# Kernel optimization log

Hardware: AMD Instinct MI355X
Metric: run time of the kernel (lower is better)

Reference implementation:

```python
import jax, jax.numpy as jnp
import numpy as np

NUM_HEADS = 8


def _attn(q, k, v, scale):
    # q: [B,H,Nq,d], k/v: [B,H,Nk,d]
    a = jax.nn.softmax(jnp.einsum('bhqd,bhkd->bhqk', q, k) * scale, axis=-1)
    return jnp.einsum('bhqk,bhkd->bhqd', a, v)


def setup_inputs() -> dict:
    key = jax.random.key(0)
    k1, k2, k3 = jax.random.split(key, 3)
    B, N, C = 8, 1024, 768
    x = jax.random.normal(k1, (B, N, C), dtype=jnp.float32)
    w_qkv = jax.random.normal(k2, (3 * C, C), dtype=jnp.float32) * 0.02
    w_proj = jax.random.normal(k3, (C, C), dtype=jnp.float32) * 0.02
    b_proj = jnp.zeros((C,), dtype=jnp.float32)
    return {"x": x, "w_qkv": w_qkv, "w_proj": w_proj, "b_proj": b_proj}


def reference(x, w_qkv, w_proj, b_proj):
    B, N, C = x.shape
    H = NUM_HEADS
    hd = C // H            # full head dim (scale uses this, per the source)
    g = hd // 3            # per-group head dim
    scale = hd ** (-0.5)

    qkv = (x @ w_qkv.T).reshape(B, N, 3, H, hd).transpose(2, 0, 3, 1, 4)  # [3,B,H,N,hd]
    q, k, v = qkv[0], qkv[1], qkv[2]

    q3, q4, q5 = q[..., :g], q[..., g:2 * g], q[..., 2 * g:]
    k3, k4, k5 = k[..., :g], k[..., g:2 * g], k[..., 2 * g:]
    v3, v4, v5 = v[..., :g], v[..., g:2 * g], v[..., 2 * g:]

    def merge(o):  # [B,H,N,g] -> [B,N,H*g]
        return o.transpose(0, 2, 1, 3).reshape(B, N, C // 3)

    x3 = merge(_attn(q4, jnp.concatenate([k3, k4], axis=2), jnp.concatenate([v3, v4], axis=2), scale))
    x4 = merge(_attn(q5, jnp.concatenate([k3, k5], axis=2), jnp.concatenate([v3, v5], axis=2), scale))
    x5 = merge(_attn(q5, jnp.concatenate([k4, k5], axis=2), jnp.concatenate([v4, v5], axis=2), scale))

    out = jnp.concatenate([x3, x4, x5], axis=2)
    return out @ w_proj.T + b_proj
```

## Files before the change

kernel.cpp:

```cpp
#include <hip/hip_runtime.h>
#include <hip/hip_bf16.h>

typedef unsigned short u16;
typedef __attribute__((ext_vector_type(8))) short short8;
typedef __attribute__((ext_vector_type(4))) float f32x4;
typedef __attribute__((ext_vector_type(4))) unsigned uint32x4;

__device__ __forceinline__ u16 f2b(float f) {
  unsigned u = __builtin_bit_cast(unsigned, f);
  unsigned r = u + 0x7fffu + ((u >> 16) & 1u);
  return (u16)(r >> 16);
}

__device__ __forceinline__ unsigned pkbf16(float lo, float hi) {
  unsigned r;
  asm("v_cvt_pk_bf16_f32 %0, %1, %2" : "=v"(r) : "v"(lo), "v"(hi));
  return r;
}

#define GLD_LDS16(gp, lp) __builtin_amdgcn_global_load_lds( \
    (const __attribute__((address_space(1))) void*)(gp),    \
    (__attribute__((address_space(3))) void*)(lp), 16, 0, 0)

__global__ __launch_bounds__(256) void cvt3(
    const float* __restrict__ x, const float* __restrict__ wq, const float* __restrict__ wp,
    u16* __restrict__ xb, u16* __restrict__ wqb, u16* __restrict__ wpb)
{
  const int NX = 8192 * 768 / 4, NQ = 2304 * 768 / 4, NP = 768 * 768 / 4;
  int i = blockIdx.x * 256 + threadIdx.x;
  if (i < NX) {
    float4 v = *(const float4*)&x[(size_t)i * 4];
    u16 o0 = f2b(v.x), o1 = f2b(v.y), o2 = f2b(v.z), o3 = f2b(v.w);
    unsigned lo = (unsigned)o0 | ((unsigned)o1 << 16);
    unsigned hi = (unsigned)o2 | ((unsigned)o3 << 16);
    uint2 pk; pk.x = lo; pk.y = hi;
    *(uint2*)&xb[(size_t)i * 4] = pk;
  } else if (i < NX + NQ) {
    int j = i - NX;
    float sc = (j < 147456) ? 0.14724447f : 1.0f;
    float4 v = *(const float4*)&wq[(size_t)j * 4];
    u16 o0 = f2b(v.x * sc), o1 = f2b(v.y * sc), o2 = f2b(v.z * sc), o3 = f2b(v.w * sc);
    uint2 pk; pk.x = (unsigned)o0 | ((unsigned)o1 << 16); pk.y = (unsigned)o2 | ((unsigned)o3 << 16);
    *(uint2*)&wqb[(size_t)j * 4] = pk;
  } else if (i < NX + NQ + NP) {
    int j = i - NX - NQ;
    int oo = (j * 4) / 768, ii = (j * 4) % 768;
    int a = ii >> 8, h = (ii >> 5) & 7, c = ii & 31;
    float4 v = *(const float4*)&wp[(size_t)j * 4];
    u16 o0 = f2b(v.x), o1 = f2b(v.y), o2 = f2b(v.z), o3 = f2b(v.w);
    uint2 pk; pk.x = (unsigned)o0 | ((unsigned)o1 << 16); pk.y = (unsigned)o2 | ((unsigned)o3 << 16);
    *(uint2*)&wpb[oo * 768 + h * 96 + a * 32 + c] = pk;
  }
}

__global__ __launch_bounds__(256) void gemm_bt(
    const u16* __restrict__ A, const u16* __restrict__ Bt,
    u16* __restrict__ Cb, float* __restrict__ Cf, const float* __restrict__ bias,
    int M, int N, int K)
{
  __shared__ u16 Al[128 * 32];
  __shared__ u16 Bl[128 * 32];
  const int tid = threadIdx.x;
  const int lane = tid & 63, wave = tid >> 6;
  const int wr = wave >> 1, wc = wave & 1;
  const int g = lane >> 4, c16 = lane & 15;
  const int m0 = blockIdx.y * 128, n0 = blockIdx.x * 128;

  f32x4 acc[4][4] = {};

  const int c0 = tid, c1 = tid + 256;
  const int r0 = c0 >> 2, o0 = (c0 & 3) * 8;
  const int r1 = c1 >> 2, o1 = (c1 & 3) * 8;
  const u16* a0 = A + (size_t)(m0 + r0) * K + o0;
  const u16* a1 = A + (size_t)(m0 + r1) * K + o1;
  const u16* b0 = Bt + (size_t)(n0 + r0) * K + o0;
  const u16* b1 = Bt + (size_t)(n0 + r1) * K + o1;

  for (int k0 = 0; k0 < K; k0 += 32) {
    GLD_LDS16(a0 + k0, Al + c0 * 8);
    GLD_LDS16(a1 + k0, Al + c1 * 8);
    GLD_LDS16(b0 + k0, Bl + c0 * 8);
    GLD_LDS16(b1 + k0, Bl + c1 * 8);
    __syncthreads();
    short8 af[4], bfr[4];
#pragma unroll
    for (int m = 0; m < 4; ++m)
      af[m] = *(const short8*)&Al[(wr * 64 + m * 16 + c16) * 32 + g * 8];
#pragma unroll
    for (int n = 0; n < 4; ++n)
      bfr[n] = *(const short8*)&Bl[(wc * 64 + n * 16 + c16) * 32 + g * 8];
#pragma unroll
    for (int m = 0; m < 4; ++m)
#pragma unroll
      for (int n = 0; n < 4; ++n)
        acc[m][n] = __builtin_amdgcn_mfma_f32_16x16x32_bf16(af[m], bfr[n], acc[m][n], 0, 0, 0);
    __syncthreads();
  }

  if (Cb) {
#pragma unroll
    for (int m = 0; m < 4; ++m) {
      const int row = m0 + wr * 64 + m * 16 + g * 4;
#pragma unroll
      for (int n = 0; n < 4; ++n) {
        const int col = n0 + wc * 64 + n * 16 + c16;
#pragma unroll
        for (int j = 0; j < 4; ++j)
          Cb[(size_t)(row + j) * N + col] = f2b(acc[m][n][j]);
      }
    }
  } else {
#pragma unroll
    for (int m = 0; m < 4; ++m) {
      const int row = m0 + wr * 64 + m * 16 + g * 4;
#pragma unroll
      for (int n = 0; n < 4; ++n) {
        const int col = n0 + wc * 64 + n * 16 + c16;
        const float bb = bias[col];
#pragma unroll
        for (int j = 0; j < 4; ++j)
          Cf[(size_t)(row + j) * N + col] = acc[m][n][j] + bb;
      }
    }
  }
}

__global__ __launch_bounds__(256) void vtrans(const u16* __restrict__ qkv, u16* __restrict__ vt)
{
  __shared__ u16 Vtl[96 * 72];
  const int tid = threadIdx.x;
  const int bh = blockIdx.x >> 4, nt = blockIdx.x & 15;
  const int b = bh >> 3, h = bh & 7;
  const int n0 = nt * 64;
  const size_t tb = (size_t)b * 1024;
#pragma unroll
  for (int i = 0; i < 3; ++i) {
    int c = tid + i * 256;
    int key = c / 12, cc = c % 12;
    short8 v = *(const short8*)&qkv[(tb + n0 + key) * 2304 + 1536 + h * 96 + cc * 8];
#pragma unroll
    for (int j = 0; j < 8; ++j)
      Vtl[(cc * 8 + j) * 72 + key] = (u16)v[j];
  }
  __syncthreads();
#pragma unroll
  for (int i = 0; i < 3; ++i) {
    int c = tid + i * 256;
    int d = c >> 3, c2 = c & 7;
    int chunk = c2 >> 2;
    int kA = ((c2 & 1) << 4) | ((c2 & 2) << 1);
    const u16* src = &Vtl[d * 72 + c2 * 8];
    size_t base = ((size_t)bh * 96 + d) * 1024 + n0 + chunk * 32;
    *(uint2*)&vt[base + kA]     = *(const uint2*)(src);
    *(uint2*)&vt[base + kA + 8] = *(const uint2*)(src + 4);
  }
}

__global__ __launch_bounds__(256, 2) void attn_kernel(
    const u16* __restrict__ qkv, const u16* __restrict__ vt, u16* __restrict__ feat)
{
  __shared__ u16 smem[3 * 64 * 40 + 96 * 72];
  u16* Kl = smem;
  u16* Vl = smem + 3 * 64 * 40;

  const int tid = threadIdx.x;
  const int lane = tid & 63, wave = tid >> 6;
  const int g = lane >> 4, c16 = lane & 15;
  const int id = blockIdx.x;
  const int h = id & 7, qt = (id >> 3) & 7, b = id >> 6;
  const int bh = b * 8 + h;
  const int q0 = qt * 128 + wave * 32;
  const size_t tb = (size_t)b * 1024;

  short8 qf[2][2];
#pragma unroll
  for (int qs = 0; qs < 2; ++qs)
#pragma unroll
    for (int m = 0; m < 2; ++m)
      qf[qs][m] = *(const short8*)&qkv[(tb + q0 + m * 16 + c16) * 2304 + h * 96 + 32 + 32 * qs + 8 * g];

  short8 ones;
#pragma unroll
  for (int i = 0; i < 8; ++i) ones[i] = (short)0x3F80;

  f32x4 acc[4][2][2] = {};
  f32x4 lsv[4][2] = {};

  int kk_key[3], kk_cc[3], vv_d[3], vv_c[3];
#pragma unroll
  for (int i = 0; i < 3; ++i) {
    int c = tid + i * 256;
    kk_key[i] = c / 12; kk_cc[i] = c % 12;
    vv_d[i] = c >> 3;   vv_c[i] = c & 7;
  }
  uint4 kst[3], vst[3];
#pragma unroll
  for (int i = 0; i < 3; ++i) {
    kst[i] = *(const uint4*)&qkv[(tb + kk_key[i]) * 2304 + 768 + h * 96 + kk_cc[i] * 8];
    vst[i] = *(const uint4*)&vt[((size_t)bh * 96 + vv_d[i]) * 1024 + vv_c[i] * 8];
  }

  const int ATT[5] = {0, 0, 1, 3, 2};
  const int QS[5]  = {0, 0, 1, 1, 1};
  const int KS[5]  = {0, 1, 0, 2, 1};

  for (int t = 0; t < 16; ++t) {
    __syncthreads();
#pragma unroll
    for (int i = 0; i < 3; ++i) {
      int part = kk_cc[i] >> 2, g4 = kk_cc[i] & 3;
      *(uint4*)&Kl[part * 2560 + kk_key[i] * 40 + g4 * 8] = kst[i];
      *(uint4*)&Vl[vv_d[i] * 72 + vv_c[i] * 8] = vst[i];
    }
    if (t < 15) {
      int kv0 = (t + 1) * 64;
#pragma unroll
      for (int i = 0; i < 3; ++i) {
        kst[i] = *(const uint4*)&qkv[(tb + kv0 + kk_key[i]) * 2304 + 768 + h * 96 + kk_cc[i] * 8];
        vst[i] = *(const uint4*)&vt[((size_t)bh * 96 + vv_d[i]) * 1024 + kv0 + vv_c[i] * 8];
      }
    }
    __syncthreads();

#pragma unroll
    for (int u = 0; u < 5; ++u) {
      const int att = ATT[u], qs = QS[u], ks = KS[u];
      short8 kf[4], vf[2][2];
#pragma unroll
      for (int n = 0; n < 4; ++n)
        kf[n] = *(const short8*)&Kl[ks * 2560 + (n * 16 + c16) * 40 + g * 8];
#pragma unroll
      for (int n = 0; n < 2; ++n)
#pragma unroll
        for (int kk = 0; kk < 2; ++kk)
          vf[n][kk] = *(const short8*)&Vl[(ks * 32 + n * 16 + c16) * 72 + kk * 32 + g * 8];

      const f32x4 z = {0.f, 0.f, 0.f, 0.f};
#pragma unroll
      for (int m = 0; m < 2; ++m) {
        f32x4 St[4];
        __builtin_amdgcn_s_setprio(1);
#pragma unroll
        for (int n = 0; n < 4; ++n)
          St[n] = __builtin_amdgcn_mfma_f32_16x16x32_bf16(kf[n], qf[qs][m], z, 0, 0, 0);
        __builtin_amdgcn_s_setprio(0);
        short8 pa[2];
#pragma unroll
        for (int kk = 0; kk < 2; ++kk) {
          uint32x4 w;
          w.x = pkbf16(__builtin_amdgcn_exp2f(St[2 * kk][0]),     __builtin_amdgcn_exp2f(St[2 * kk][1]));
          w.y = pkbf16(__builtin_amdgcn_exp2f(St[2 * kk][2]),     __builtin_amdgcn_exp2f(St[2 * kk][3]));
          w.z = pkbf16(__builtin_amdgcn_exp2f(St[2 * kk + 1][0]), __builtin_amdgcn_exp2f(St[2 * kk + 1][1]));
          w.w = pkbf16(__builtin_amdgcn_exp2f(St[2 * kk + 1][2]), __builtin_amdgcn_exp2f(St[2 * kk + 1][3]));
          pa[kk] = __builtin_bit_cast(short8, w);
        }
        __builtin_amdgcn_s_setprio(1);
#pragma unroll
        for (int n = 0; n < 2; ++n)
#pragma unroll
          for (int kk = 0; kk < 2; ++kk)
            acc[att][m][n] = __builtin_amdgcn_mfma_f32_16x16x32_bf16(pa[kk], vf[n][kk], acc[att][m][n], 0, 0, 0);
#pragma unroll
        for (int kk = 0; kk < 2; ++kk)
          lsv[att][m] = __builtin_amdgcn_mfma_f32_16x16x32_bf16(pa[kk], ones, lsv[att][m], 0, 0, 0);
        __builtin_amdgcn_s_setprio(0);
      }
    }
  }

#pragma unroll
  for (int m = 0; m < 2; ++m) {
    lsv[1][m] += lsv[3][m];
    lsv[2][m] += lsv[3][m];
#pragma unroll
    for (int n = 0; n < 2; ++n) {
      acc[1][m][n] += acc[3][m][n];
      acc[2][m][n] += acc[3][m][n];
    }
  }

  __syncthreads();
  u16* Ol = smem + wave * 3072;
#pragma unroll
  for (int a = 0; a < 3; ++a)
#pragma unroll
    for (int m = 0; m < 2; ++m) {
      f32x4 inv;
#pragma unroll
      for (int r = 0; r < 4; ++r) inv[r] = 1.0f / lsv[a][m][r];
#pragma unroll
      for (int n = 0; n < 2; ++n)
#pragma unroll
        for (int r = 0; r < 4; ++r)
          Ol[(m * 16 + g * 4 + r) * 96 + a * 32 + n * 16 + c16] = f2b(acc[a][m][n][r] * inv[r]);
    }
  __builtin_amdgcn_s_barrier();
#pragma unroll
  for (int i = 0; i < 6; ++i) {
    int chunk = lane + 64 * i;
    int row = chunk / 12, cc = chunk % 12;
    uint4 val = *(const uint4*)&Ol[row * 96 + cc * 8];
    *(uint4*)&feat[(tb + q0 + row) * 768 + h * 96 + cc * 8] = val;
  }
}

extern "C" void kernel_launch(void* const* d_in, const int* in_sizes, int n_in,
                              void* d_out, int out_size, void* d_ws, size_t ws_size,
                              hipStream_t stream) {
  const float* x  = (const float*)d_in[0];
  const float* wq = (const float*)d_in[1];
  const float* wp = (const float*)d_in[2];
  const float* bp = (const float*)d_in[3];
  float* out = (float*)d_out;

  char* ws = (char*)d_ws;
  u16* xb    = (u16*)(ws);
  u16* wqb   = (u16*)(ws + 12582912);
  u16* wpb   = (u16*)(ws + 16121856);
  u16* qkvb  = (u16*)(ws + 17301504);
  u16* vtb   = (u16*)(ws + 55050240);
  u16* featb = xb;

  cvt3<<<8448, 256, 0, stream>>>(x, wq, wp, xb, wqb, wpb);
  gemm_bt<<<dim3(18, 64), 256, 0, stream>>>(xb, wqb, qkvb, nullptr, nullptr, 8192, 2304, 768);
  vtrans<<<1024, 256, 0, stream>>>(qkvb, vtb);
  attn_kernel<<<512, 256, 0, stream>>>(qkvb, vtb, featb);
  gemm_bt<<<dim3(6, 64), 256, 0, stream>>>(featb, wpb, nullptr, out, bp, 8192, 768, 768);
}
```

Measured before the change: 167.1 us.

## Fuse V transpose into QKV GEMM epilogue and split attention per output group

The QKV GEMM epilogue now writes V tiles directly in the transposed, permuted layout the attention kernel expects, which removes the separate vtrans kernel and its extra read and write of V. The attention kernel is split so each block handles one of the three output groups (1536 blocks instead of 512). This drops the shared-k/v accumulation trick, so the total MFMA work rises from 5 to 6 units per tile, but each block uses fewer registers and less LDS and the launch bound allows 5 blocks per CU for occupancy. The float-to-bf16 conversion kernel also switches to the packed hardware convert instruction.

```diff
diff --git a/kernel.cpp b/kernel.cpp
--- a/kernel.cpp
+++ b/kernel.cpp
@@ -30,25 +30,20 @@
   int i = blockIdx.x * 256 + threadIdx.x;
   if (i < NX) {
     float4 v = *(const float4*)&x[(size_t)i * 4];
-    u16 o0 = f2b(v.x), o1 = f2b(v.y), o2 = f2b(v.z), o3 = f2b(v.w);
-    unsigned lo = (unsigned)o0 | ((unsigned)o1 << 16);
-    unsigned hi = (unsigned)o2 | ((unsigned)o3 << 16);
-    uint2 pk; pk.x = lo; pk.y = hi;
+    uint2 pk; pk.x = pkbf16(v.x, v.y); pk.y = pkbf16(v.z, v.w);
     *(uint2*)&xb[(size_t)i * 4] = pk;
   } else if (i < NX + NQ) {
     int j = i - NX;
     float sc = (j < 147456) ? 0.14724447f : 1.0f;
     float4 v = *(const float4*)&wq[(size_t)j * 4];
-    u16 o0 = f2b(v.x * sc), o1 = f2b(v.y * sc), o2 = f2b(v.z * sc), o3 = f2b(v.w * sc);
-    uint2 pk; pk.x = (unsigned)o0 | ((unsigned)o1 << 16); pk.y = (unsigned)o2 | ((unsigned)o3 << 16);
+    uint2 pk; pk.x = pkbf16(v.x * sc, v.y * sc); pk.y = pkbf16(v.z * sc, v.w * sc);
     *(uint2*)&wqb[(size_t)j * 4] = pk;
   } else if (i < NX + NQ + NP) {
     int j = i - NX - NQ;
     int oo = (j * 4) / 768, ii = (j * 4) % 768;
     int a = ii >> 8, h = (ii >> 5) & 7, c = ii & 31;
     float4 v = *(const float4*)&wp[(size_t)j * 4];
-    u16 o0 = f2b(v.x), o1 = f2b(v.y), o2 = f2b(v.z), o3 = f2b(v.w);
-    uint2 pk; pk.x = (unsigned)o0 | ((unsigned)o1 << 16); pk.y = (unsigned)o2 | ((unsigned)o3 << 16);
+    uint2 pk; pk.x = pkbf16(v.x, v.y); pk.y = pkbf16(v.z, v.w);
     *(uint2*)&wpb[oo * 768 + h * 96 + a * 32 + c] = pk;
   }
 }
@@ -56,7 +51,7 @@
 __global__ __launch_bounds__(256) void gemm_bt(
     const u16* __restrict__ A, const u16* __restrict__ Bt,
     u16* __restrict__ Cb, float* __restrict__ Cf, const float* __restrict__ bias,
-    int M, int N, int K)
+    u16* __restrict__ vt_out, int M, int N, int K)
 {
   __shared__ u16 Al[128 * 32];
   __shared__ u16 Bl[128 * 32];
@@ -98,15 +93,34 @@
   }
 
   if (Cb) {
-#pragma unroll
-    for (int m = 0; m < 4; ++m) {
-      const int row = m0 + wr * 64 + m * 16 + g * 4;
-#pragma unroll
-      for (int n = 0; n < 4; ++n) {
-        const int col = n0 + wc * 64 + n * 16 + c16;
-#pragma unroll
-        for (int j = 0; j < 4; ++j)
-          Cb[(size_t)(row + j) * N + col] = f2b(acc[m][n][j]);
+    if (vt_out && n0 >= 1536) {
+#pragma unroll
+      for (int m = 0; m < 4; ++m) {
+        const int row0 = m0 + wr * 64 + m * 16 + g * 4;
+        const int bb = row0 >> 10, nb = row0 & 1023;
+        const int chunk = nb & ~31, o = nb & 31;
+        const int slot0 = ((o >> 2) & 3) * 8 + ((o >> 4) & 1) * 4;
+#pragma unroll
+        for (int n = 0; n < 4; ++n) {
+          const int colg = n0 - 1536 + wc * 64 + n * 16 + c16;
+          const int hh = colg / 96, dd = colg % 96;
+          uint2 pk;
+          pk.x = pkbf16(acc[m][n][0], acc[m][n][1]);
+          pk.y = pkbf16(acc[m][n][2], acc[m][n][3]);
+          *(uint2*)&vt_out[((size_t)(bb * 8 + hh) * 96 + dd) * 1024 + chunk + slot0] = pk;
+        }
+      }
+    } else {
+#pragma unroll
+      for (int m = 0; m < 4; ++m) {
+        const int row = m0 + wr * 64 + m * 16 + g * 4;
+#pragma unroll
+        for (int n = 0; n < 4; ++n) {
+          const int col = n0 + wc * 64 + n * 16 + c16;
+#pragma unroll
+          for (int j = 0; j < 4; ++j)
+            Cb[(size_t)(row + j) * N + col] = f2b(acc[m][n][j]);
+        }
       }
     }
   } else {
@@ -125,115 +139,80 @@
   }
 }
 
-__global__ __launch_bounds__(256) void vtrans(const u16* __restrict__ qkv, u16* __restrict__ vt)
-{
-  __shared__ u16 Vtl[96 * 72];
-  const int tid = threadIdx.x;
-  const int bh = blockIdx.x >> 4, nt = blockIdx.x & 15;
-  const int b = bh >> 3, h = bh & 7;
-  const int n0 = nt * 64;
-  const size_t tb = (size_t)b * 1024;
-#pragma unroll
-  for (int i = 0; i < 3; ++i) {
-    int c = tid + i * 256;
-    int key = c / 12, cc = c % 12;
-    short8 v = *(const short8*)&qkv[(tb + n0 + key) * 2304 + 1536 + h * 96 + cc * 8];
-#pragma unroll
-    for (int j = 0; j < 8; ++j)
-      Vtl[(cc * 8 + j) * 72 + key] = (u16)v[j];
-  }
-  __syncthreads();
-#pragma unroll
-  for (int i = 0; i < 3; ++i) {
-    int c = tid + i * 256;
-    int d = c >> 3, c2 = c & 7;
-    int chunk = c2 >> 2;
-    int kA = ((c2 & 1) << 4) | ((c2 & 2) << 1);
-    const u16* src = &Vtl[d * 72 + c2 * 8];
-    size_t base = ((size_t)bh * 96 + d) * 1024 + n0 + chunk * 32;
-    *(uint2*)&vt[base + kA]     = *(const uint2*)(src);
-    *(uint2*)&vt[base + kA + 8] = *(const uint2*)(src + 4);
-  }
-}
-
-__global__ __launch_bounds__(256, 2) void attn_kernel(
+__global__ __launch_bounds__(256, 5) void attn_kernel(
     const u16* __restrict__ qkv, const u16* __restrict__ vt, u16* __restrict__ feat)
 {
-  __shared__ u16 smem[3 * 64 * 40 + 96 * 72];
+  __shared__ u16 smem[2 * 2560 + 64 * 72];
   u16* Kl = smem;
-  u16* Vl = smem + 3 * 64 * 40;
+  u16* Vl = smem + 2 * 2560;
 
   const int tid = threadIdx.x;
   const int lane = tid & 63, wave = tid >> 6;
   const int g = lane >> 4, c16 = lane & 15;
   const int id = blockIdx.x;
-  const int h = id & 7, qt = (id >> 3) & 7, b = id >> 6;
+  const int h = id & 7;
+  const int r3 = id >> 3;
+  const int aidx = r3 % 3;
+  const int t2 = r3 / 3;
+  const int qt = t2 & 7, b = t2 >> 3;
   const int bh = b * 8 + h;
   const int q0 = qt * 128 + wave * 32;
   const size_t tb = (size_t)b * 1024;
 
-  short8 qf[2][2];
-#pragma unroll
-  for (int qs = 0; qs < 2; ++qs)
-#pragma unroll
-    for (int m = 0; m < 2; ++m)
-      qf[qs][m] = *(const short8*)&qkv[(tb + q0 + m * 16 + c16) * 2304 + h * 96 + 32 + 32 * qs + 8 * g];
+  const int p0 = (aidx == 2) ? 1 : 0;
+  const int p1 = (aidx == 0) ? 1 : 2;
+  const int qoff = (aidx == 0) ? 32 : 64;
+
+  short8 qf[2];
+#pragma unroll
+  for (int m = 0; m < 2; ++m)
+    qf[m] = *(const short8*)&qkv[(tb + q0 + m * 16 + c16) * 2304 + h * 96 + qoff + 8 * g];
 
   short8 ones;
 #pragma unroll
   for (int i = 0; i < 8; ++i) ones[i] = (short)0x3F80;
 
-  f32x4 acc[4][2][2] = {};
-  f32x4 lsv[4][2] = {};
-
-  int kk_key[3], kk_cc[3], vv_d[3], vv_c[3];
-#pragma unroll
-  for (int i = 0; i < 3; ++i) {
-    int c = tid + i * 256;
-    kk_key[i] = c / 12; kk_cc[i] = c % 12;
-    vv_d[i] = c >> 3;   vv_c[i] = c & 7;
-  }
-  uint4 kst[3], vst[3];
-#pragma unroll
-  for (int i = 0; i < 3; ++i) {
-    kst[i] = *(const uint4*)&qkv[(tb + kk_key[i]) * 2304 + 768 + h * 96 + kk_cc[i] * 8];
-    vst[i] = *(const uint4*)&vt[((size_t)bh * 96 + vv_d[i]) * 1024 + vv_c[i] * 8];
-  }
-
-  const int ATT[5] = {0, 0, 1, 3, 2};
-  const int QS[5]  = {0, 0, 1, 1, 1};
-  const int KS[5]  = {0, 1, 0, 2, 1};
+  f32x4 acc[2][2] = {};
+  f32x4 lsv[2] = {};
+
+  const int kkey = tid >> 2, kcc = tid & 3;
+  const int vd = tid >> 3, vc = tid & 7;
+  const int P[2] = { p0, p1 };
+  uint4 kst[2], vst[2];
+#pragma unroll
+  for (int i = 0; i < 2; ++i) {
+    kst[i] = *(const uint4*)&qkv[(tb + kkey) * 2304 + 768 + h * 96 + P[i] * 32 + kcc * 8];
+    vst[i] = *(const uint4*)&vt[((size_t)bh * 96 + P[i] * 32 + vd) * 1024 + vc * 8];
+  }
 
   for (int t = 0; t < 16; ++t) {
     __syncthreads();
 #pragma unroll
-    for (int i = 0; i < 3; ++i) {
-      int part = kk_cc[i] >> 2, g4 = kk_cc[i] & 3;
-      *(uint4*)&Kl[part * 2560 + kk_key[i] * 40 + g4 * 8] = kst[i];
-      *(uint4*)&Vl[vv_d[i] * 72 + vv_c[i] * 8] = vst[i];
+    for (int i = 0; i < 2; ++i) {
+      *(uint4*)&Kl[i * 2560 + kkey * 40 + kcc * 8] = kst[i];
+      *(uint4*)&Vl[(i * 32 + vd) * 72 + vc * 8] = vst[i];
     }
     if (t < 15) {
       int kv0 = (t + 1) * 64;
 #pragma unroll
-      for (int i = 0; i < 3; ++i) {
-        kst[i] = *(const uint4*)&qkv[(tb + kv0 + kk_key[i]) * 2304 + 768 + h * 96 + kk_cc[i] * 8];
-        vst[i] = *(const uint4*)&vt[((size_t)bh * 96 + vv_d[i]) * 1024 + kv0 + vv_c[i] * 8];
-      }
-    }
-    __syncthreads();
-
-#pragma unroll
-    for (int u = 0; u < 5; ++u) {
-      const int att = ATT[u], qs = QS[u], ks = KS[u];
+      for (int i = 0; i < 2; ++i) {
+        kst[i] = *(const uint4*)&qkv[(tb + kv0 + kkey) * 2304 + 768 + h * 96 + P[i] * 32 + kcc * 8];
+        vst[i] = *(const uint4*)&vt[((size_t)bh * 96 + P[i] * 32 + vd) * 1024 + kv0 + vc * 8];
+      }
+    }
+    __syncthreads();
+
+#pragma unroll
+    for (int u = 0; u < 2; ++u) {
       short8 kf[4], vf[2][2];
 #pragma unroll
       for (int n = 0; n < 4; ++n)
-        kf[n] = *(const short8*)&Kl[ks * 2560 + (n * 16 + c16) * 40 + g * 8];
+        kf[n] = *(const short8*)&Kl[u * 2560 + (n * 16 + c16) * 40 + g * 8];
 #pragma unroll
       for (int n = 0; n < 2; ++n)
 #pragma unroll
         for (int kk = 0; kk < 2; ++kk)
-          vf[n][kk] = *(const short8*)&Vl[(ks * 32 + n * 16 + c16) * 72 + kk * 32 + g * 8];
+          vf[n][kk] = *(const short8*)&Vl[(u * 32 + n * 16 + c16) * 72 + kk * 32 + g * 8];
 
       const f32x4 z = {0.f, 0.f, 0.f, 0.f};
 #pragma unroll
@@ -242,7 +221,7 @@
         __builtin_amdgcn_s_setprio(1);
 #pragma unroll
         for (int n = 0; n < 4; ++n)
-          St[n] = __builtin_amdgcn_mfma_f32_16x16x32_bf16(kf[n], qf[qs][m], z, 0, 0, 0);
+          St[n] = __builtin_amdgcn_mfma_f32_16x16x32_bf16(kf[n], qf[m], z, 0, 0, 0);
         __builtin_amdgcn_s_setprio(0);
         short8 pa[2];
 #pragma unroll
@@ -259,48 +238,34 @@
         for (int n = 0; n < 2; ++n)
 #pragma unroll
           for (int kk = 0; kk < 2; ++kk)
-            acc[att][m][n] = __builtin_amdgcn_mfma_f32_16x16x32_bf16(pa[kk], vf[n][kk], acc[att][m][n], 0, 0, 0);
+            acc[m][n] = __builtin_amdgcn_mfma_f32_16x16x32_bf16(pa[kk], vf[n][kk], acc[m][n], 0, 0, 0);
 #pragma unroll
         for (int kk = 0; kk < 2; ++kk)
-          lsv[att][m] = __builtin_amdgcn_mfma_f32_16x16x32_bf16(pa[kk], ones, lsv[att][m], 0, 0, 0);
+          lsv[m] = __builtin_amdgcn_mfma_f32_16x16x32_bf16(pa[kk], ones, lsv[m], 0, 0, 0);
         __builtin_amdgcn_s_setprio(0);
       }
     }
   }
 
+  __syncthreads();
+  u16* Ol = smem + wave * 1024;
 #pragma unroll
   for (int m = 0; m < 2; ++m) {
-    lsv[1][m] += lsv[3][m];
-    lsv[2][m] += lsv[3][m];
-#pragma unroll
-    for (int n = 0; n < 2; ++n) {
-      acc[1][m][n] += acc[3][m][n];
-      acc[2][m][n] += acc[3][m][n];
-    }
-  }
-
-  __syncthreads();
-  u16* Ol = smem + wave * 3072;
-#pragma unroll
-  for (int a = 0; a < 3; ++a)
-#pragma unroll
-    for (int m = 0; m < 2; ++m) {
-      f32x4 inv;
-#pragma unroll
-      for (int r = 0; r < 4; ++r) inv[r] = 1.0f / lsv[a][m][r];
-#pragma unroll
-      for (int n = 0; n < 2; ++n)
-#pragma unroll
-        for (int r = 0; r < 4; ++r)
-          Ol[(m * 16 + g * 4 + r) * 96 + a * 32 + n * 16 + c16] = f2b(acc[a][m][n][r] * inv[r]);
-    }
-  __builtin_amdgcn_s_barrier();
-#pragma unroll
-  for (int i = 0; i < 6; ++i) {
-    int chunk = lane + 64 * i;
-    int row = chunk / 12, cc = chunk % 12;
-    uint4 val = *(const uint4*)&Ol[row * 96 + cc * 8];
-    *(uint4*)&feat[(tb + q0 + row) * 768 + h * 96 + cc * 8] = val;
+    f32x4 inv;
+#pragma unroll
+    for (int r = 0; r < 4; ++r) inv[r] = 1.0f / lsv[m][r];
+#pragma unroll
+    for (int n = 0; n < 2; ++n)
+#pragma unroll
+      for (int r = 0; r < 4; ++r)
+        Ol[(m * 16 + g * 4 + r) * 32 + n * 16 + c16] = f2b(acc[m][n][r] * inv[r]);
+  }
+#pragma unroll
+  for (int i = 0; i < 2; ++i) {
+    int idx = lane + 64 * i;
+    int row = idx >> 2, q4 = idx & 3;
+    uint4 val = *(const uint4*)&Ol[row * 32 + q4 * 8];
+    *(uint4*)&feat[(tb + q0 + row) * 768 + h * 96 + aidx * 32 + q4 * 8] = val;
   }
 }
 
@@ -322,8 +287,7 @@
   u16* featb = xb;
 
   cvt3<<<8448, 256, 0, stream>>>(x, wq, wp, xb, wqb, wpb);
-  gemm_bt<<<dim3(18, 64), 256, 0, stream>>>(xb, wqb, qkvb, nullptr, nullptr, 8192, 2304, 768);
-  vtrans<<<1024, 256, 0, stream>>>(qkvb, vtb);
-  attn_kernel<<<512, 256, 0, stream>>>(qkvb, vtb, featb);
-  gemm_bt<<<dim3(6, 64), 256, 0, stream>>>(featb, wpb, nullptr, out, bp, 8192, 768, 768);
-}
+  gemm_bt<<<dim3(18, 64), 256, 0, stream>>>(xb, wqb, qkvb, nullptr, nullptr, vtb, 8192, 2304, 768);
+  attn_kernel<<<1536, 256, 0, stream>>>(qkvb, vtb, featb);
+  gemm_bt<<<dim3(6, 64), 256, 0, stream>>>(featb, wpb, nullptr, out, bp, nullptr, 8192, 768, 768);
+}
```

Measured after the change: 204.9 us. 1.23x slower.
